# Kernel tuning notes

Hardware: AMD Instinct MI355X
Metric: run time of the kernel (lower is better)

## Reference

```python
import jax, jax.numpy as jnp
import numpy as np

HIDDEN = 2048
N_HEADS = 8
N_KV_HEADS = 1
HEAD_DIM = 256
ROPE_THETA = 10000.0
B, S = 2, 2048


def setup_inputs() -> dict:
    key = jax.random.key(0)
    ks = jax.random.split(key, 6)
    sc = 0.02
    hidden_states = jax.random.normal(ks[0], (B, S, HIDDEN), dtype=jnp.float32)
    position_ids = jnp.broadcast_to(jnp.arange(S, dtype=jnp.int64 if jax.config.jax_enable_x64 else jnp.int32), (B, S))
    # additive causal mask: 0 on/below diagonal, large negative above
    causal = jnp.tril(jnp.ones((S, S), dtype=bool))
    attention_mask = jnp.where(causal, 0.0, -1e9).astype(jnp.float32)[None, None, :, :]
    attention_mask = jnp.broadcast_to(attention_mask, (B, 1, S, S))
    Wq = jax.random.normal(ks[1], (HIDDEN, N_HEADS * HEAD_DIM), dtype=jnp.float32) * sc
    Wk = jax.random.normal(ks[2], (HIDDEN, N_KV_HEADS * HEAD_DIM), dtype=jnp.float32) * sc
    Wv = jax.random.normal(ks[3], (HIDDEN, N_KV_HEADS * HEAD_DIM), dtype=jnp.float32) * sc
    Wo = jax.random.normal(ks[4], (N_HEADS * HEAD_DIM, HIDDEN), dtype=jnp.float32) * sc
    return {"hidden_states": hidden_states, "position_ids": position_ids,
            "attention_mask": attention_mask, "Wq": Wq, "Wk": Wk, "Wv": Wv, "Wo": Wo}


def _rotate_half(x):
    x1, x2 = jnp.split(x, 2, axis=-1)
    return jnp.concatenate([-x2, x1], axis=-1)


def _rope_cos_sin(position_ids, dtype):
    # inv_freq: [head_dim/2]
    inv_freq = 1.0 / (ROPE_THETA ** (jnp.arange(0, HEAD_DIM, 2, dtype=jnp.float32) / HEAD_DIM))
    # freqs: [B, S, head_dim/2]
    freqs = position_ids.astype(jnp.float32)[:, :, None] * inv_freq[None, None, :]
    emb = jnp.concatenate([freqs, freqs], axis=-1)  # [B, S, head_dim]
    return jnp.cos(emb).astype(dtype), jnp.sin(emb).astype(dtype)


def reference(hidden_states, position_ids, attention_mask, Wq, Wk, Wv, Wo):
    b, s, _ = hidden_states.shape
    # projections (bias=False)
    q = (hidden_states @ Wq).reshape(b, s, N_HEADS, HEAD_DIM).transpose(0, 2, 1, 3)      # [B,H,S,D]
    k = (hidden_states @ Wk).reshape(b, s, N_KV_HEADS, HEAD_DIM).transpose(0, 2, 1, 3)   # [B,Hk,S,D]
    v = (hidden_states @ Wv).reshape(b, s, N_KV_HEADS, HEAD_DIM).transpose(0, 2, 1, 3)
    cos, sin = _rope_cos_sin(position_ids, hidden_states.dtype)  # [B,S,D]
    cos, sin = cos[:, None], sin[:, None]  # [B,1,S,D]
    q = q * cos + _rotate_half(q) * sin
    k = k * cos + _rotate_half(k) * sin
    # repeat_kv for GQA
    n_rep = N_HEADS // N_KV_HEADS
    k = jnp.repeat(k, n_rep, axis=1)  # [B,H,S,D]
    v = jnp.repeat(v, n_rep, axis=1)
    scale = HEAD_DIM ** -0.5
    scores = jnp.einsum('bhqd,bhkd->bhqk', q, k) * scale + attention_mask
    attn_weights = jax.nn.softmax(scores.astype(jnp.float32), axis=-1).astype(q.dtype)
    attn_out = jnp.einsum('bhqk,bhkd->bhqd', attn_weights, v)
    attn_out = attn_out.transpose(0, 2, 1, 3).reshape(b, s, N_HEADS * HEAD_DIM)
    out = attn_out @ Wo
    return out, attn_weights
```

## Files before the change

kernel.cpp:

```cpp
#include <hip/hip_runtime.h>
#include <hip/hip_bf16.h>
#include <math.h>

typedef __attribute__((ext_vector_type(4))) float f32x4;
typedef __attribute__((ext_vector_type(8))) __bf16 bf16x8;
typedef __attribute__((ext_vector_type(8))) unsigned short u16x8;
typedef __attribute__((ext_vector_type(4))) unsigned short u16x4;

#define HID    2048
#define NHEADS 8
#define HDIM   256
#define SEQ    2048
#define BATCH  2
#define ROWS   (BATCH*SEQ)
#define QKVN   (NHEADS*HDIM + 2*HDIM)
#define NBH    (BATCH*NHEADS)

typedef __attribute__((address_space(1))) const void gvoid_t;
typedef __attribute__((address_space(3))) void lvoid_t;

__device__ __forceinline__ void gload16(const void* g, void* l){
  __builtin_amdgcn_global_load_lds((gvoid_t*)g, (lvoid_t*)l, 16, 0, 0);
}

__device__ __forceinline__ float bf2f(unsigned short u){
  union { unsigned int i; float f; } x; x.i = ((unsigned int)u) << 16; return x.f;
}
__device__ __forceinline__ unsigned short f2bf(float f){
  union { float f; unsigned int i; } x; x.f = f;
  unsigned int u = x.i;
  return (unsigned short)((u + 0x7FFFu + ((u >> 16) & 1u)) >> 16);
}

__global__ __launch_bounds__(256)
void k_f32_to_bf16(const float* __restrict__ src, unsigned short* __restrict__ dst){
  long i = ((long)blockIdx.x * 256 + threadIdx.x) * 16;
  f32x4 x0 = *(const f32x4*)(src + i);
  f32x4 x1 = *(const f32x4*)(src + i + 4);
  f32x4 x2 = *(const f32x4*)(src + i + 8);
  f32x4 x3 = *(const f32x4*)(src + i + 12);
  u16x8 w0, w1;
  #pragma unroll
  for (int j = 0; j < 4; ++j){
    w0[j]   = f2bf(x0[j]);
    w0[4+j] = f2bf(x1[j]);
    w1[j]   = f2bf(x2[j]);
    w1[4+j] = f2bf(x3[j]);
  }
  *(u16x8*)(dst + i)     = w0;
  *(u16x8*)(dst + i + 8) = w1;
}

__global__ __launch_bounds__(256)
void k_transpose(const float* __restrict__ src, unsigned short* __restrict__ dst,
                 int srcCols, int dstLd){
  __shared__ float t[32][33];
  int bx = blockIdx.x * 32;
  int by = blockIdx.y * 32;
  int tx = threadIdx.x & 31, ty = threadIdx.x >> 5;
  #pragma unroll
  for (int i = 0; i < 4; ++i){
    int rr = ty + i*8;
    t[rr][tx] = src[(long)(by + rr)*srcCols + bx + tx];
  }
  __syncthreads();
  #pragma unroll
  for (int i = 0; i < 4; ++i){
    int rr = ty + i*8;
    dst[(long)(bx + rr)*dstLd + by + tx] = f2bf(t[tx][rr]);
  }
}

__global__ __launch_bounds__(256)
void k_rope(const unsigned short* __restrict__ qkv, const int* __restrict__ pos_ids,
            unsigned short* __restrict__ Qb, unsigned short* __restrict__ Kb){
  int row = blockIdx.x;
  float pos = (float)pos_ids[row];
  int tid = threadIdx.x;
  const unsigned short* r = qkv + (long)row * QKVN;

  #pragma unroll
  for (int it = 0; it < 4; ++it){
    int p = it*256 + tid;
    int d = p & 127, h = p >> 7;
    int col = h*HDIM + d;
    float inv = exp2f((float)d * -0.10381025296523132f);
    float ang = pos * inv;
    float sn, cs; sincosf(ang, &sn, &cs);
    float x0 = bf2f(r[col]), x1 = bf2f(r[col + 128]);
    Qb[(long)row*HID + col]       = f2bf(x0*cs - x1*sn);
    Qb[(long)row*HID + col + 128] = f2bf(x1*cs + x0*sn);
  }
  if (tid < 128){
    int d = tid;
    float inv = exp2f((float)d * -0.10381025296523132f);
    float ang = pos * inv;
    float sn, cs; sincosf(ang, &sn, &cs);
    float x0 = bf2f(r[HID + d]), x1 = bf2f(r[HID + d + 128]);
    Kb[(long)row*HDIM + d]       = f2bf(x0*cs - x1*sn);
    Kb[(long)row*HDIM + d + 128] = f2bf(x1*cs + x0*sn);
  }
}

__global__ __launch_bounds__(256)
void k_vt(const unsigned short* __restrict__ qkvb, unsigned short* __restrict__ VT){
  __shared__ unsigned short t[32][34];
  int d0 = blockIdx.x * 32, s0 = blockIdx.y * 32, b = blockIdx.z;
  int tx = threadIdx.x & 31, ty = threadIdx.x >> 5;
  #pragma unroll
  for (int i = 0; i < 4; ++i){
    int rr = ty + i*8;
    t[rr][tx] = qkvb[(long)(b*SEQ + s0 + rr)*QKVN + HID + HDIM + d0 + tx];
  }
  __syncthreads();
  #pragma unroll
  for (int i = 0; i < 4; ++i){
    int dd = ty + i*8;
    VT[((long)b*HDIM + d0 + dd)*SEQ + s0 + tx] = t[tx][dd];
  }
}

__global__ __launch_bounds__(512, 4)
void k_fused(const unsigned short* __restrict__ Qb, const unsigned short* __restrict__ Kb,
             const unsigned short* __restrict__ VT, float* __restrict__ S,
             unsigned short* __restrict__ AOb){
  int bh = blockIdx.x, b = bh >> 3, h = bh & 7;
  int ss = 31 - (int)blockIdx.y;
  int qbase = ss * 64;
  int T = 2 * (ss + 1);

  float* Sh = S + (long)bh * SEQ * SEQ;
  const unsigned short* Qh = Qb + (long)b*SEQ*HID + (long)h*HDIM;
  const unsigned short* Kh = Kb + (long)b*SEQ*HDIM;
  const unsigned short* Vh = VT + (long)b*HDIM*SEQ;

  __shared__ unsigned short lQ[64*256];
  __shared__ unsigned short lK[2][32*256];
  __shared__ unsigned short lA[64*40];
  __shared__ float lWl[8][64];
  __shared__ float mli[64];

  int tid = threadIdx.x, lane = tid & 63, w = tid >> 6;
  int wr = w >> 1, wc = w & 1;

#define STAGE_Q                                                                 \
  { _Pragma("unroll")                                                           \
    for (int t = 0; t < 4; ++t){                                                \
      int seg = w*4 + t;                                                        \
      int row = seg*2 + (lane >> 5);                                            \
      int cb  = ((lane & 31)*16) ^ ((row & 7) << 4);                            \
      gload16(Qh + (long)(qbase + row)*HID + (cb >> 1), (char*)lQ + seg*1024);  \
    } }

#define STAGE_K(kt_, buf_)                                                      \
  { _Pragma("unroll")                                                           \
    for (int t = 0; t < 2; ++t){                                                \
      int seg = w*2 + t;                                                        \
      int row = seg*2 + (lane >> 5);                                            \
      int cb  = ((lane & 31)*16) ^ ((row & 7) << 4);                            \
      gload16(Kh + (long)((kt_)*32 + row)*HDIM + (cb >> 1),                     \
              (char*)lK[buf_] + seg*1024);                                      \
    } }

#define QKT(buf_)                                                               \
  { _Pragma("unroll")                                                           \
    for (int kk = 0; kk < 8; ++kk){                                             \
      int rk = wc*16 + (lane & 15);                                             \
      bf16x8 bk = *(const bf16x8*)((const char*)lK[buf_] + rk*512 +             \
                   ((kk*64 + (lane >> 4)*16) ^ ((rk & 7) << 4)));               \
      int rq = wr*16 + (lane & 15);                                             \
      bf16x8 aq = *(const bf16x8*)((const char*)lQ + rq*512 +                   \
                   ((kk*64 + (lane >> 4)*16) ^ ((rq & 7) << 4)));               \
      accs = __builtin_amdgcn_mfma_f32_16x16x32_bf16(aq, bk, accs, 0, 0, 0);    \
    } }

  f32x4 accs;
  f32x4 acc_o[4][2];
  float oL[4];
  #pragma unroll
  for (int q = 0; q < 4; ++q){ accs[q] = 0.f; oL[q] = 0.f; }
  #pragma unroll
  for (int m = 0; m < 4; ++m)
    #pragma unroll
    for (int n = 0; n < 2; ++n)
      #pragma unroll
      for (int q = 0; q < 4; ++q) acc_o[m][n][q] = 0.f;

  STAGE_Q
  STAGE_K(0, 0)
  STAGE_K(1, 1)
  for (int kt = 0; kt < T; ++kt){
    bf16x8 vf0 = *(const bf16x8*)(Vh + (long)(w*32 +      (lane & 15))*SEQ + kt*32 + (lane >> 4)*8);
    bf16x8 vf1 = *(const bf16x8*)(Vh + (long)(w*32 + 16 + (lane & 15))*SEQ + kt*32 + (lane >> 4)*8);
    asm volatile("s_waitcnt vmcnt(4)" ::: "memory");
    __builtin_amdgcn_s_barrier();
    __builtin_amdgcn_s_setprio(1);
    QKT(kt & 1)
    __builtin_amdgcn_s_setprio(0);
    #pragma unroll
    for (int ri = 0; ri < 4; ++ri){
      int rowl = wr*16 + (lane >> 4)*4 + ri;
      int coll = wc*16 + (lane & 15);
      float e = (kt*32 + coll <= qbase + rowl) ? __expf(accs[ri]*0.0625f - 8.0f) : 0.f;
      oL[ri] += e;
      lA[rowl*40 + coll] = f2bf(e);
      accs[ri] = 0.f;
    }
    asm volatile("s_waitcnt lgkmcnt(0)" ::: "memory");
    __builtin_amdgcn_s_barrier();
    if (kt + 2 < T) STAGE_K(kt + 2, kt & 1)
    __builtin_amdgcn_s_setprio(1);
    #pragma unroll
    for (int m2 = 0; m2 < 4; ++m2){
      int rq = m2*16 + (lane & 15);
      bf16x8 ap = *(const bf16x8*)&lA[rq*40 + (lane >> 4)*8];
      acc_o[m2][0] = __builtin_amdgcn_mfma_f32_16x16x32_bf16(ap, vf0, acc_o[m2][0], 0, 0, 0);
      acc_o[m2][1] = __builtin_amdgcn_mfma_f32_16x16x32_bf16(ap, vf1, acc_o[m2][1], 0, 0, 0);
    }
    __builtin_amdgcn_s_setprio(0);
  }

  #pragma unroll
  for (int ri = 0; ri < 4; ++ri){
    float v = oL[ri];
    #pragma unroll
    for (int off = 1; off < 16; off <<= 1) v += __shfl_xor(v, off);
    if ((lane & 15) == 0)
      lWl[w][wr*16 + (lane >> 4)*4 + ri] = v;
  }
  __syncthreads();
  if (tid < 64){
    int g = (tid >> 4) * 2;
    mli[tid] = 1.0f / (lWl[g][tid] + lWl[g+1][tid]);
  }
  __syncthreads();

  float ils[4], ilo[4][4];
  #pragma unroll
  for (int ri = 0; ri < 4; ++ri)
    ils[ri] = mli[wr*16 + (lane >> 4)*4 + ri];
  #pragma unroll
  for (int m2 = 0; m2 < 4; ++m2)
    #pragma unroll
    for (int ri = 0; ri < 4; ++ri)
      ilo[m2][ri] = mli[m2*16 + (lane >> 4)*4 + ri];

  #pragma unroll
  for (int m2 = 0; m2 < 4; ++m2){
    #pragma unroll
    for (int ri = 0; ri < 4; ++ri){
      int row = qbase + m2*16 + (lane >> 4)*4 + ri;
      long gr = (long)b*SEQ + row;
      #pragma unroll
      for (int n = 0; n < 2; ++n){
        int col = w*32 + n*16 + (lane & 15);
        AOb[gr*HID + h*HDIM + col] = f2bf(acc_o[m2][n][ri] * ilo[m2][ri]);
      }
    }
  }

  STAGE_K(0, 0)
  STAGE_K(1, 1)
  for (int kt = 0; kt < T; ++kt){
    if (kt == 0)           asm volatile("s_waitcnt vmcnt(2)" ::: "memory");
    else if (kt + 1 >= T)  asm volatile("s_waitcnt vmcnt(1)" ::: "memory");
    else                   asm volatile("s_waitcnt vmcnt(4)" ::: "memory");
    __builtin_amdgcn_s_barrier();
    __builtin_amdgcn_s_setprio(1);
    QKT(kt & 1)
    __builtin_amdgcn_s_setprio(0);
    #pragma unroll
    for (int ri = 0; ri < 4; ++ri){
      int rowl = wr*16 + (lane >> 4)*4 + ri;
      int coll = wc*16 + (lane & 15);
      float p = (kt*32 + coll <= qbase + rowl)
                ? __expf(accs[ri]*0.0625f - 8.0f) * ils[ri] : 0.f;
      lA[rowl*40 + coll] = f2bf(p);
      accs[ri] = 0.f;
    }
    asm volatile("s_waitcnt lgkmcnt(0)" ::: "memory");
    __builtin_amdgcn_s_barrier();
    if (kt + 2 < T) STAGE_K(kt + 2, kt & 1)
    {
      int row = tid >> 3, l8 = tid & 7;
      u16x4 v = *(const u16x4*)&lA[row*40 + l8*4];
      f32x4 o;
      #pragma unroll
      for (int j = 0; j < 4; ++j) o[j] = bf2f(v[j]);
      *(f32x4*)&Sh[(long)(qbase + row)*SEQ + kt*32 + l8*4] = o;
    }
  }

  {
    f32x4 z4; z4[0]=0.f; z4[1]=0.f; z4[2]=0.f; z4[3]=0.f;
    int row = qbase + (tid >> 3);
    for (int c = T*32 + (tid & 7)*4; c < SEQ; c += 32)
      *(f32x4*)&Sh[(long)row*SEQ + c] = z4;
  }
#undef STAGE_Q
#undef STAGE_K
#undef QKT
}

template<int OUTF32>
__global__ __launch_bounds__(512, 1)
void gemm256(const unsigned short* __restrict__ A16, const unsigned short* __restrict__ BT,
             void* __restrict__ Cv, int lda, int ldb, int ldc, int K){
  constexpr int BM = 256, BN = 128, BK = 64;
  int m0 = blockIdx.x * BM, n0 = blockIdx.y * BN;

  __shared__ unsigned short lA[2][BM*BK];
  __shared__ unsigned short lB[2][BN*BK];

  int tid = threadIdx.x, lane = tid & 63, w = tid >> 6;
  int wr = w >> 1, wc = w & 1;
  int srow = lane >> 3;
  int vswz = ((lane & 7) ^ ((lane >> 3) & 7)) * 8;

  f32x4 acc[4][4];
  #pragma unroll
  for (int m = 0; m < 4; ++m)
    #pragma unroll
    for (int n = 0; n < 4; ++n)
      #pragma unroll
      for (int q = 0; q < 4; ++q) acc[m][n][q] = 0.f;

  int NT = K / BK;

#define STAGE256(kt_, buf_)                                                    \
  { int k0_ = (kt_) * BK;                                                      \
    _Pragma("unroll")                                                          \
    for (int t = 0; t < 4; ++t){                                               \
      int seg = w*4 + t;                                                       \
      const unsigned short* src = A16 + (long)(m0 + seg*8 + srow)*lda + k0_ + vswz; \
      gload16(src, (char*)lA[buf_] + seg*1024);                                \
    }                                                                          \
    _Pragma("unroll")                                                          \
    for (int t = 0; t < 2; ++t){                                               \
      int seg = w*2 + t;                                                       \
      const unsigned short* src = BT + (long)(n0 + seg*8 + srow)*ldb + k0_ + vswz; \
      gload16(src, (char*)lB[buf_] + seg*1024);                                \
    } }

  STAGE256(0, 0)
  STAGE256(1, 1)
  int cur = 0;

  for (int kt = 0; kt < NT; ++kt){
    if (kt < NT - 1) asm volatile("s_waitcnt vmcnt(6)" ::: "memory");
    else             asm volatile("s_waitcnt vmcnt(0)" ::: "memory");
    __builtin_amdgcn_s_barrier();

    const char* La = (const char*)lA[cur];
    const char* Lb = (const char*)lB[cur];
    __builtin_amdgcn_s_setprio(1);
    #pragma unroll
    for (int kk = 0; kk < 2; ++kk){
      bf16x8 af[4], bfr[4];
      #pragma unroll
      for (int m = 0; m < 4; ++m){
        int row = wr*64 + m*16 + (lane & 15);
        int kb = (kk*64 + (lane >> 4)*16) ^ ((row & 7) << 4);
        af[m] = *(const bf16x8*)(La + row*128 + kb);
      }
      #pragma unroll
      for (int n = 0; n < 4; ++n){
        int row = wc*64 + n*16 + (lane & 15);
        int kb = (kk*64 + (lane >> 4)*16) ^ ((row & 7) << 4);
        bfr[n] = *(const bf16x8*)(Lb + row*128 + kb);
      }
      #pragma unroll
      for (int m = 0; m < 4; ++m)
        #pragma unroll
        for (int n = 0; n < 4; ++n)
          acc[m][n] = __builtin_amdgcn_mfma_f32_16x16x32_bf16(af[m], bfr[n], acc[m][n], 0, 0, 0);
    }
    __builtin_amdgcn_s_setprio(0);
    __builtin_amdgcn_s_barrier();
    if (kt + 2 < NT) STAGE256(kt + 2, cur)
    cur ^= 1;
  }
#undef STAGE256

  #pragma unroll
  for (int m = 0; m < 4; ++m){
    #pragma unroll
    for (int ri = 0; ri < 4; ++ri){
      int orow = m0 + wr*64 + m*16 + (lane >> 4)*4 + ri;
      #pragma unroll
      for (int n = 0; n < 4; ++n){
        int ocol = n0 + wc*64 + n*16 + (lane & 15);
        float vv = acc[m][n][ri];
        if (OUTF32) ((float*)Cv)[(long)orow*ldc + ocol] = vv;
        else        ((unsigned short*)Cv)[(long)orow*ldc + ocol] = f2bf(vv);
      }
    }
  }
}

extern "C" void kernel_launch(void* const* d_in, const int* in_sizes, int n_in,
                              void* d_out, int out_size, void* d_ws, size_t ws_size,
                              hipStream_t stream){
  const float* hs  = (const float*)d_in[0];
  const int*   pos = (const int*)  d_in[1];
  const float* Wq  = (const float*)d_in[3];
  const float* Wk  = (const float*)d_in[4];
  const float* Wv  = (const float*)d_in[5];
  const float* Wo  = (const float*)d_in[6];

  float* out  = (float*)d_out;
  float* Sbuf = out + (long)ROWS * HID;

  unsigned short* wsp   = (unsigned short*)d_ws;
  unsigned short* hsb   = wsp;
  unsigned short* wqkvT = hsb   + (long)ROWS*HID;
  unsigned short* woT   = wqkvT + (long)QKVN*HID;
  unsigned short* qkvb  = woT   + (long)HID*HID;
  unsigned short* Qb    = qkvb  + (long)ROWS*QKVN;
  unsigned short* Kb    = Qb    + (long)ROWS*HID;
  unsigned short* VT    = Kb    + (long)ROWS*HDIM;
  unsigned short* AOb   = VT    + (long)BATCH*HDIM*SEQ;

  k_f32_to_bf16<<<(ROWS*HID)/(256*16), 256, 0, stream>>>(hs, hsb);
  k_transpose<<<dim3(HID/32,  HID/32), 256, 0, stream>>>(Wq, wqkvT, HID, HID);
  k_transpose<<<dim3(HDIM/32, HID/32), 256, 0, stream>>>(Wk, wqkvT + (long)HID*HID, HDIM, HID);
  k_transpose<<<dim3(HDIM/32, HID/32), 256, 0, stream>>>(Wv, wqkvT + (long)(HID+HDIM)*HID, HDIM, HID);
  k_transpose<<<dim3(HID/32,  HID/32), 256, 0, stream>>>(Wo, woT, HID, HID);

  gemm256<0><<<dim3(ROWS/256, QKVN/128), 512, 0, stream>>>(
      hsb, wqkvT, qkvb, HID, HID, QKVN, HID);

  k_rope<<<ROWS, 256, 0, stream>>>(qkvb, pos, Qb, Kb);
  k_vt<<<dim3(HDIM/32, SEQ/32, BATCH), 256, 0, stream>>>(qkvb, VT);

  k_fused<<<dim3(NBH, 32), 512, 0, stream>>>(Qb, Kb, VT, Sbuf, AOb);

  gemm256<1><<<dim3(ROWS/256, HID/128), 512, 0, stream>>>(
      AOb, woT, out, HID, HID, HID, HID);
}
```

Before: 342.3 us.

## Hold Q fragments in registers and double-buffer P tile to cut barriers

Q fragments are loaded straight into registers instead of staging them in LDS, which frees 32KB of shared memory. The P tile in LDS is now double-buffered, so each iteration needs one fewer barrier, and the V loads are issued after the softmax step. The second pass writes probabilities straight from registers to global memory rather than bouncing them through LDS. This drops the bf16 rounding of the stored attention weights but makes the stores scattered rather than 16-byte vectorized. The vmcnt wait counts were reworked to match, which is fragile when STAGE_K is skipped near the end of the loop.

```diff
diff --git a/kernel.cpp b/kernel.cpp
--- a/kernel.cpp
+++ b/kernel.cpp
@@ -134,23 +134,13 @@
   const unsigned short* Kh = Kb + (long)b*SEQ*HDIM;
   const unsigned short* Vh = VT + (long)b*HDIM*SEQ;
 
-  __shared__ unsigned short lQ[64*256];
   __shared__ unsigned short lK[2][32*256];
-  __shared__ unsigned short lA[64*40];
+  __shared__ unsigned short lA[2][64*40];
   __shared__ float lWl[8][64];
   __shared__ float mli[64];
 
   int tid = threadIdx.x, lane = tid & 63, w = tid >> 6;
   int wr = w >> 1, wc = w & 1;
-
-#define STAGE_Q                                                                 \
-  { _Pragma("unroll")                                                           \
-    for (int t = 0; t < 4; ++t){                                                \
-      int seg = w*4 + t;                                                        \
-      int row = seg*2 + (lane >> 5);                                            \
-      int cb  = ((lane & 31)*16) ^ ((row & 7) << 4);                            \
-      gload16(Qh + (long)(qbase + row)*HID + (cb >> 1), (char*)lQ + seg*1024);  \
-    } }
 
 #define STAGE_K(kt_, buf_)                                                      \
   { _Pragma("unroll")                                                           \
@@ -168,11 +158,16 @@
       int rk = wc*16 + (lane & 15);                                             \
       bf16x8 bk = *(const bf16x8*)((const char*)lK[buf_] + rk*512 +             \
                    ((kk*64 + (lane >> 4)*16) ^ ((rk & 7) << 4)));               \
-      int rq = wr*16 + (lane & 15);                                             \
-      bf16x8 aq = *(const bf16x8*)((const char*)lQ + rq*512 +                   \
-                   ((kk*64 + (lane >> 4)*16) ^ ((rq & 7) << 4)));               \
-      accs = __builtin_amdgcn_mfma_f32_16x16x32_bf16(aq, bk, accs, 0, 0, 0);    \
+      accs = __builtin_amdgcn_mfma_f32_16x16x32_bf16(aq[kk], bk, accs, 0, 0, 0);\
     } }
+
+  bf16x8 aq[8];
+  {
+    const unsigned short* qrow = Qh + (long)(qbase + wr*16 + (lane & 15))*HID + (lane >> 4)*8;
+    #pragma unroll
+    for (int kk = 0; kk < 8; ++kk)
+      aq[kk] = *(const bf16x8*)(qrow + kk*32);
+  }
 
   f32x4 accs;
   f32x4 acc_o[4][2];
@@ -186,14 +181,11 @@
       #pragma unroll
       for (int q = 0; q < 4; ++q) acc_o[m][n][q] = 0.f;
 
-  STAGE_Q
   STAGE_K(0, 0)
   STAGE_K(1, 1)
+  asm volatile("s_waitcnt vmcnt(2)" ::: "memory");
+  __builtin_amdgcn_s_barrier();
   for (int kt = 0; kt < T; ++kt){
-    bf16x8 vf0 = *(const bf16x8*)(Vh + (long)(w*32 +      (lane & 15))*SEQ + kt*32 + (lane >> 4)*8);
-    bf16x8 vf1 = *(const bf16x8*)(Vh + (long)(w*32 + 16 + (lane & 15))*SEQ + kt*32 + (lane >> 4)*8);
-    asm volatile("s_waitcnt vmcnt(4)" ::: "memory");
-    __builtin_amdgcn_s_barrier();
     __builtin_amdgcn_s_setprio(1);
     QKT(kt & 1)
     __builtin_amdgcn_s_setprio(0);
@@ -203,17 +195,20 @@
       int coll = wc*16 + (lane & 15);
       float e = (kt*32 + coll <= qbase + rowl) ? __expf(accs[ri]*0.0625f - 8.0f) : 0.f;
       oL[ri] += e;
-      lA[rowl*40 + coll] = f2bf(e);
+      lA[kt & 1][rowl*40 + coll] = f2bf(e);
       accs[ri] = 0.f;
     }
+    bf16x8 vf0 = *(const bf16x8*)(Vh + (long)(w*32 +      (lane & 15))*SEQ + kt*32 + (lane >> 4)*8);
+    bf16x8 vf1 = *(const bf16x8*)(Vh + (long)(w*32 + 16 + (lane & 15))*SEQ + kt*32 + (lane >> 4)*8);
     asm volatile("s_waitcnt lgkmcnt(0)" ::: "memory");
+    asm volatile("s_waitcnt vmcnt(2)" ::: "memory");
     __builtin_amdgcn_s_barrier();
     if (kt + 2 < T) STAGE_K(kt + 2, kt & 1)
     __builtin_amdgcn_s_setprio(1);
     #pragma unroll
     for (int m2 = 0; m2 < 4; ++m2){
       int rq = m2*16 + (lane & 15);
-      bf16x8 ap = *(const bf16x8*)&lA[rq*40 + (lane >> 4)*8];
+      bf16x8 ap = *(const bf16x8*)&lA[kt & 1][rq*40 + (lane >> 4)*8];
       acc_o[m2][0] = __builtin_amdgcn_mfma_f32_16x16x32_bf16(ap, vf0, acc_o[m2][0], 0, 0, 0);
       acc_o[m2][1] = __builtin_amdgcn_mfma_f32_16x16x32_bf16(ap, vf1, acc_o[m2][1], 0, 0, 0);
     }
@@ -235,37 +230,31 @@
   }
   __syncthreads();
 
-  float ils[4], ilo[4][4];
+  float ils[4];
   #pragma unroll
   for (int ri = 0; ri < 4; ++ri)
     ils[ri] = mli[wr*16 + (lane >> 4)*4 + ri];
-  #pragma unroll
-  for (int m2 = 0; m2 < 4; ++m2)
-    #pragma unroll
-    for (int ri = 0; ri < 4; ++ri)
-      ilo[m2][ri] = mli[m2*16 + (lane >> 4)*4 + ri];
 
   #pragma unroll
   for (int m2 = 0; m2 < 4; ++m2){
     #pragma unroll
     for (int ri = 0; ri < 4; ++ri){
-      int row = qbase + m2*16 + (lane >> 4)*4 + ri;
-      long gr = (long)b*SEQ + row;
+      int row = m2*16 + (lane >> 4)*4 + ri;
+      float il = mli[row];
+      long gr = (long)b*SEQ + qbase + row;
       #pragma unroll
       for (int n = 0; n < 2; ++n){
         int col = w*32 + n*16 + (lane & 15);
-        AOb[gr*HID + h*HDIM + col] = f2bf(acc_o[m2][n][ri] * ilo[m2][ri]);
+        AOb[gr*HID + h*HDIM + col] = f2bf(acc_o[m2][n][ri] * il);
       }
     }
   }
 
   STAGE_K(0, 0)
   STAGE_K(1, 1)
+  asm volatile("s_waitcnt vmcnt(2)" ::: "memory");
+  __builtin_amdgcn_s_barrier();
   for (int kt = 0; kt < T; ++kt){
-    if (kt == 0)           asm volatile("s_waitcnt vmcnt(2)" ::: "memory");
-    else if (kt + 1 >= T)  asm volatile("s_waitcnt vmcnt(1)" ::: "memory");
-    else                   asm volatile("s_waitcnt vmcnt(4)" ::: "memory");
-    __builtin_amdgcn_s_barrier();
     __builtin_amdgcn_s_setprio(1);
     QKT(kt & 1)
     __builtin_amdgcn_s_setprio(0);
@@ -275,20 +264,12 @@
       int coll = wc*16 + (lane & 15);
       float p = (kt*32 + coll <= qbase + rowl)
                 ? __expf(accs[ri]*0.0625f - 8.0f) * ils[ri] : 0.f;
-      lA[rowl*40 + coll] = f2bf(p);
+      Sh[(long)(qbase + rowl)*SEQ + kt*32 + coll] = p;
       accs[ri] = 0.f;
     }
-    asm volatile("s_waitcnt lgkmcnt(0)" ::: "memory");
+    asm volatile("s_waitcnt vmcnt(4)" ::: "memory");
     __builtin_amdgcn_s_barrier();
     if (kt + 2 < T) STAGE_K(kt + 2, kt & 1)
-    {
-      int row = tid >> 3, l8 = tid & 7;
-      u16x4 v = *(const u16x4*)&lA[row*40 + l8*4];
-      f32x4 o;
-      #pragma unroll
-      for (int j = 0; j < 4; ++j) o[j] = bf2f(v[j]);
-      *(f32x4*)&Sh[(long)(qbase + row)*SEQ + kt*32 + l8*4] = o;
-    }
   }
 
   {
@@ -297,7 +278,6 @@
     for (int c = T*32 + (tid & 7)*4; c < SEQ; c += 32)
       *(f32x4*)&Sh[(long)row*SEQ + c] = z4;
   }
-#undef STAGE_Q
 #undef STAGE_K
 #undef QKT
 }
```

Result: faster. 318.3 us (-7.0%).
